# Performance work log

Measured on AMD Instinct MI355X. Metric: run time of the kernel, lower is better.

Reference implementation:

```python
import jax, jax.numpy as jnp
import numpy as np

PS = 8  # patch_size


def setup_inputs() -> dict:
    key = jax.random.key(0)
    k1, k2 = jax.random.split(key)
    shape = (16, 3, 512, 512)
    return {
        "input": jax.random.normal(k1, shape, dtype=jnp.float32),
        "target": jax.random.normal(k2, shape, dtype=jnp.float32),
    }


def _extract_patches(x):
    # (B,C,H,W) -> (B,C,nh,nw,ps,ps); H,W assumed divisible by PS (no pad needed)
    B, C, H, W = x.shape
    x = x.reshape(B, C, H // PS, PS, W // PS, PS)
    return jnp.transpose(x, (0, 1, 2, 4, 3, 5))


def _fft_feats(patches):
    fft = jnp.fft.fft2(patches, norm="ortho")          # over last two axes
    fft = jnp.fft.fftshift(fft, axes=(-2, -1))
    real, imag = fft.real, fft.imag
    # log1p norm: sign(x) * log1p(|x|)
    real = jnp.sign(real) * jnp.log1p(jnp.abs(real))
    imag = jnp.sign(imag) * jnp.log1p(jnp.abs(imag))
    return real, imag


def reference(input, target):
    ir, ii = _fft_feats(_extract_patches(input))
    tr, ti = _fft_feats(_extract_patches(target))
    loss = (ir - tr) ** 2 + (ii - ti) ** 2   # mse real + mse imag, unreduced
    return jnp.mean(loss)
```

## Files before the change

kernel.cpp:

```cpp
#include <hip/hip_runtime.h>

#define SQ1_2 0.70710678118654752440f

__device__ __forceinline__ float g_feat(float x) {
    return copysignf(__logf(1.0f + fabsf(x)), x);
}

__device__ __forceinline__ void rfft8(const float r[8], float o[8]) {
    float s0 = r[0] + r[4], d0 = r[0] - r[4];
    float s1 = r[1] + r[5], d1 = r[1] - r[5];
    float s2 = r[2] + r[6], d2 = r[2] - r[6];
    float s3 = r[3] + r[7], d3 = r[3] - r[7];
    float ss02 = s0 + s2, sd02 = s0 - s2;
    float ss13 = s1 + s3, sd13 = s1 - s3;
    float t1 = SQ1_2 * (d1 - d3);
    float t2 = SQ1_2 * (d1 + d3);
    o[0] = ss02 + ss13;
    o[1] = ss02 - ss13;
    o[2] = d0 + t1;
    o[3] = -(d2 + t2);
    o[4] = sd02;
    o[5] = -sd13;
    o[6] = d0 - t1;
    o[7] = d2 - t2;
}

__device__ __forceinline__ void cfft8(const float xr[8], const float xi[8],
                                      float Fr[8], float Fi[8]) {
    float s0r = xr[0] + xr[4], s0i = xi[0] + xi[4], d0r = xr[0] - xr[4], d0i = xi[0] - xi[4];
    float s1r = xr[1] + xr[5], s1i = xi[1] + xi[5], d1r = xr[1] - xr[5], d1i = xi[1] - xi[5];
    float s2r = xr[2] + xr[6], s2i = xi[2] + xi[6], d2r = xr[2] - xr[6], d2i = xi[2] - xi[6];
    float s3r = xr[3] + xr[7], s3i = xi[3] + xi[7], d3r = xr[3] - xr[7], d3i = xi[3] - xi[7];
    float ss0r = s0r + s2r, ss0i = s0i + s2i, sd0r = s0r - s2r, sd0i = s0i - s2i;
    float ss1r = s1r + s3r, ss1i = s1i + s3i, sd1r = s1r - s3r, sd1i = s1i - s3i;
    Fr[0] = ss0r + ss1r; Fi[0] = ss0i + ss1i;
    Fr[4] = ss0r - ss1r; Fi[4] = ss0i - ss1i;
    Fr[2] = sd0r + sd1i; Fi[2] = sd0i - sd1r;
    Fr[6] = sd0r - sd1i; Fi[6] = sd0i + sd1r;
    float t1r = SQ1_2 * (d1r + d1i), t1i = SQ1_2 * (d1i - d1r);
    float t2r = d2i,                 t2i = -d2r;
    float t3r = SQ1_2 * (d3i - d3r), t3i = -SQ1_2 * (d3r + d3i);
    float ts0r = d0r + t2r, ts0i = d0i + t2i, td0r = d0r - t2r, td0i = d0i - t2i;
    float ts1r = t1r + t3r, ts1i = t1i + t3i, td1r = t1r - t3r, td1i = t1i - t3i;
    Fr[1] = ts0r + ts1r; Fi[1] = ts0i + ts1i;
    Fr[5] = ts0r - ts1r; Fi[5] = ts0i - ts1i;
    Fr[3] = td0r + td1i; Fi[3] = td0i - td1r;
    Fr[7] = td0r - td1i; Fi[7] = td0i + td1r;
}

__device__ __forceinline__ void stage1(const float* __restrict__ src, long base,
                                       float v[64]) {
    #pragma unroll
    for (int m = 0; m < 8; ++m) {
        const float4* p = reinterpret_cast<const float4*>(src + base + (long)m * 512);
        float4 a = p[0];
        float4 b = p[1];
        float r[8] = {a.x * 0.125f, a.y * 0.125f, a.z * 0.125f, a.w * 0.125f,
                      b.x * 0.125f, b.y * 0.125f, b.z * 0.125f, b.w * 0.125f};
        rfft8(r, &v[m * 8]);
    }
}

__device__ __forceinline__ void stage2_feats(const float v[64], float f[64]) {
    #pragma unroll
    for (int j = 0; j < 2; ++j) {
        float c[8], o[8];
        #pragma unroll
        for (int m = 0; m < 8; ++m) c[m] = v[m * 8 + j];
        rfft8(c, o);
        #pragma unroll
        for (int k = 0; k < 8; ++k) f[j * 8 + k] = g_feat(o[k]);
    }
    #pragma unroll
    for (int l = 0; l < 3; ++l) {
        float cr[8], ci[8], Fr[8], Fi[8];
        #pragma unroll
        for (int m = 0; m < 8; ++m) {
            cr[m] = v[m * 8 + 2 + 2 * l];
            ci[m] = v[m * 8 + 3 + 2 * l];
        }
        cfft8(cr, ci, Fr, Fi);
        #pragma unroll
        for (int k = 0; k < 8; ++k) {
            f[16 + l * 16 + k]     = g_feat(Fr[k]);
            f[16 + l * 16 + 8 + k] = g_feat(Fi[k]);
        }
    }
}

__global__ __launch_bounds__(256) void patchfft_loss_kernel(
        const float* __restrict__ in, const float* __restrict__ tgt,
        float* __restrict__ out) {
    int p = blockIdx.x * 256 + threadIdx.x;
    int pw = p & 63;
    int ph = (p >> 6) & 63;
    int bc = p >> 12;
    long base = (long)bc * 262144 + ph * 4096 + pw * 8;

    float a[64];
    stage1(in, base, a);
    float f[64];
    stage2_feats(a, f);

    stage1(tgt, base, a);

    float acc1 = 0.0f, acc2 = 0.0f;
    #pragma unroll
    for (int j = 0; j < 2; ++j) {
        float c[8], o[8];
        #pragma unroll
        for (int m = 0; m < 8; ++m) c[m] = a[m * 8 + j];
        rfft8(c, o);
        {
            float d0 = f[j * 8 + 0] - g_feat(o[0]); acc1 += d0 * d0;
            float d1 = f[j * 8 + 1] - g_feat(o[1]); acc1 += d1 * d1;
        }
        #pragma unroll
        for (int k = 2; k < 8; ++k) {
            float d = f[j * 8 + k] - g_feat(o[k]); acc2 += d * d;
        }
    }
    #pragma unroll
    for (int l = 0; l < 3; ++l) {
        float cr[8], ci[8], Fr[8], Fi[8];
        #pragma unroll
        for (int m = 0; m < 8; ++m) {
            cr[m] = a[m * 8 + 2 + 2 * l];
            ci[m] = a[m * 8 + 3 + 2 * l];
        }
        cfft8(cr, ci, Fr, Fi);
        #pragma unroll
        for (int k = 0; k < 8; ++k) {
            float d = f[16 + l * 16 + k]     - g_feat(Fr[k]); acc2 += d * d;
            float e = f[16 + l * 16 + 8 + k] - g_feat(Fi[k]); acc2 += e * e;
        }
    }
    float loss = acc1 + 2.0f * acc2;

    #pragma unroll
    for (int off = 32; off > 0; off >>= 1) loss += __shfl_down(loss, off, 64);
    __shared__ float wsum[4];
    int lane = threadIdx.x & 63;
    int wid  = threadIdx.x >> 6;
    if (lane == 0) wsum[wid] = loss;
    __syncthreads();
    if (threadIdx.x == 0) {
        float s = wsum[0] + wsum[1] + wsum[2] + wsum[3];
        atomicAdd(out, s * (1.0f / 12582912.0f));
    }
}

extern "C" void kernel_launch(void* const* d_in, const int* in_sizes, int n_in,
                              void* d_out, int out_size, void* d_ws, size_t ws_size,
                              hipStream_t stream) {
    const float* in  = (const float*)d_in[0];
    const float* tgt = (const float*)d_in[1];
    float* out = (float*)d_out;
    (void)in_sizes; (void)n_in; (void)d_ws; (void)ws_size; (void)out_size;

    hipMemsetAsync(out, 0, sizeof(float), stream);
    patchfft_loss_kernel<<<768, 256, 0, stream>>>(in, tgt, out);
}
```

Measured before the change: 120.5 us.

## Split input and target patches across wavefront halves, combine via cross-lane shuffle

```diff
diff --git a/kernel.cpp b/kernel.cpp
--- a/kernel.cpp
+++ b/kernel.cpp
@@ -48,20 +48,32 @@
     Fr[7] = td0r - td1i; Fi[7] = td0i + td1r;
 }
 
-__device__ __forceinline__ void stage1(const float* __restrict__ src, long base,
-                                       float v[64]) {
+__global__ __launch_bounds__(256, 5) void patchfft_loss_kernel(
+        const float* __restrict__ in, const float* __restrict__ tgt,
+        float* __restrict__ out) {
+    int t = blockIdx.x * 256 + threadIdx.x;
+    int lane = t & 63;
+    int w = t >> 6;
+    int pi = w * 32 + (lane & 31);
+    const float* src = (lane >= 32) ? tgt : in;
+
+    int pw = pi & 63;
+    int ph = (pi >> 6) & 63;
+    int bc = pi >> 12;
+    long base = (long)bc * 262144 + ph * 4096 + pw * 8;
+
+    float v[64];
     #pragma unroll
     for (int m = 0; m < 8; ++m) {
-        const float4* p = reinterpret_cast<const float4*>(src + base + (long)m * 512);
-        float4 a = p[0];
-        float4 b = p[1];
-        float r[8] = {a.x * 0.125f, a.y * 0.125f, a.z * 0.125f, a.w * 0.125f,
-                      b.x * 0.125f, b.y * 0.125f, b.z * 0.125f, b.w * 0.125f};
+        const float4* p4 = reinterpret_cast<const float4*>(src + base + (long)m * 512);
+        float4 a0 = p4[0];
+        float4 a1 = p4[1];
+        float r[8] = {a0.x * 0.125f, a0.y * 0.125f, a0.z * 0.125f, a0.w * 0.125f,
+                      a1.x * 0.125f, a1.y * 0.125f, a1.z * 0.125f, a1.w * 0.125f};
         rfft8(r, &v[m * 8]);
     }
-}
 
-__device__ __forceinline__ void stage2_feats(const float v[64], float f[64]) {
+    float acc1 = 0.0f, acc2 = 0.0f;
     #pragma unroll
     for (int j = 0; j < 2; ++j) {
         float c[8], o[8];
@@ -69,7 +81,12 @@
         for (int m = 0; m < 8; ++m) c[m] = v[m * 8 + j];
         rfft8(c, o);
         #pragma unroll
-        for (int k = 0; k < 8; ++k) f[j * 8 + k] = g_feat(o[k]);
+        for (int k = 0; k < 8; ++k) {
+            float fm = g_feat(o[k]);
+            float d = fm - __shfl_xor(fm, 32, 64);
+            if (k < 2) acc1 += d * d;
+            else       acc2 += d * d;
+        }
     }
     #pragma unroll
     for (int l = 0; l < 3; ++l) {
@@ -82,57 +99,11 @@
         cfft8(cr, ci, Fr, Fi);
         #pragma unroll
         for (int k = 0; k < 8; ++k) {
-            f[16 + l * 16 + k]     = g_feat(Fr[k]);
-            f[16 + l * 16 + 8 + k] = g_feat(Fi[k]);
-        }
-    }
-}
-
-__global__ __launch_bounds__(256) void patchfft_loss_kernel(
-        const float* __restrict__ in, const float* __restrict__ tgt,
-        float* __restrict__ out) {
-    int p = blockIdx.x * 256 + threadIdx.x;
-    int pw = p & 63;
-    int ph = (p >> 6) & 63;
-    int bc = p >> 12;
-    long base = (long)bc * 262144 + ph * 4096 + pw * 8;
-
-    float a[64];
-    stage1(in, base, a);
-    float f[64];
-    stage2_feats(a, f);
-
-    stage1(tgt, base, a);
-
-    float acc1 = 0.0f, acc2 = 0.0f;
-    #pragma unroll
-    for (int j = 0; j < 2; ++j) {
-        float c[8], o[8];
-        #pragma unroll
-        for (int m = 0; m < 8; ++m) c[m] = a[m * 8 + j];
-        rfft8(c, o);
-        {
-            float d0 = f[j * 8 + 0] - g_feat(o[0]); acc1 += d0 * d0;
-            float d1 = f[j * 8 + 1] - g_feat(o[1]); acc1 += d1 * d1;
-        }
-        #pragma unroll
-        for (int k = 2; k < 8; ++k) {
-            float d = f[j * 8 + k] - g_feat(o[k]); acc2 += d * d;
-        }
-    }
-    #pragma unroll
-    for (int l = 0; l < 3; ++l) {
-        float cr[8], ci[8], Fr[8], Fi[8];
-        #pragma unroll
-        for (int m = 0; m < 8; ++m) {
-            cr[m] = a[m * 8 + 2 + 2 * l];
-            ci[m] = a[m * 8 + 3 + 2 * l];
-        }
-        cfft8(cr, ci, Fr, Fi);
-        #pragma unroll
-        for (int k = 0; k < 8; ++k) {
-            float d = f[16 + l * 16 + k]     - g_feat(Fr[k]); acc2 += d * d;
-            float e = f[16 + l * 16 + 8 + k] - g_feat(Fi[k]); acc2 += e * e;
+            float fr = g_feat(Fr[k]);
+            float fi = g_feat(Fi[k]);
+            float dr = fr - __shfl_xor(fr, 32, 64);
+            float di = fi - __shfl_xor(fi, 32, 64);
+            acc2 += dr * dr + di * di;
         }
     }
     float loss = acc1 + 2.0f * acc2;
@@ -140,13 +111,12 @@
     #pragma unroll
     for (int off = 32; off > 0; off >>= 1) loss += __shfl_down(loss, off, 64);
     __shared__ float wsum[4];
-    int lane = threadIdx.x & 63;
-    int wid  = threadIdx.x >> 6;
-    if (lane == 0) wsum[wid] = loss;
+    int wid = threadIdx.x >> 6;
+    if ((threadIdx.x & 63) == 0) wsum[wid] = loss;
     __syncthreads();
     if (threadIdx.x == 0) {
         float s = wsum[0] + wsum[1] + wsum[2] + wsum[3];
-        atomicAdd(out, s * (1.0f / 12582912.0f));
+        atomicAdd(out, s * (1.0f / 25165824.0f));
     }
 }
 
@@ -159,5 +129,5 @@
     (void)in_sizes; (void)n_in; (void)d_ws; (void)ws_size; (void)out_size;
 
     hipMemsetAsync(out, 0, sizeof(float), stream);
-    patchfft_loss_kernel<<<768, 256, 0, stream>>>(in, tgt, out);
+    patchfft_loss_kernel<<<1536, 256, 0, stream>>>(in, tgt, out);
 }
```

Result: slower. 124.2 us (+3.0%).
